# Performance work log

Measured on AMD Instinct MI355X. Metric: run time of the kernel, lower is better.

Reference implementation:

```python
import jax, jax.numpy as jnp
import numpy as np

EC = 64        # n_elts
N = 262144     # number of sample points (2048 rays * 128 samples)


def setup_inputs() -> dict:
    key = jax.random.key(0)
    ks = jax.random.split(key, 7)
    return {
        "world_space_points": jax.random.uniform(ks[0], (N, 3), minval=-0.7, maxval=0.7, dtype=jnp.float32),
        "nerflet_activations": jax.random.normal(ks[1], (EC, N, 4), dtype=jnp.float32),
        "dists": jax.random.uniform(ks[2], (N, 1), minval=0.0, maxval=0.1, dtype=jnp.float32),
        "constants": jax.random.uniform(ks[3], (EC, 1), minval=5.0, maxval=5.1, dtype=jnp.float32),
        "centers": jax.random.uniform(ks[4], (EC, 3), minval=-0.6, maxval=0.6, dtype=jnp.float32),
        "radii": jax.random.uniform(ks[5], (EC, 3), minval=0.05, maxval=0.06, dtype=jnp.float32),
        "rotations": jax.random.uniform(ks[6], (EC, 3), minval=-np.pi, maxval=np.pi, dtype=jnp.float32),
    }


def _rotation_matrices(rpy):
    # rpy: [EC, 3] roll-pitch-yaw -> [EC, 3, 3]
    c = jnp.cos(rpy)
    s = jnp.sin(rpy)
    cx, cy, cz = c[..., 0], c[..., 1], c[..., 2]
    sx, sy, sz = s[..., 0], s[..., 1], s[..., 2]
    R = jnp.stack([
        cz * cy, cz * sy * sx - sz * cx, cz * sy * cx + sz * sx,
        sz * cy, sz * sy * sx + cz * cx, sz * sy * cx - cz * sx,
        -sy,     cy * sx,                cy * cx,
    ], axis=-1)
    return R.reshape(rpy.shape[:-1] + (3, 3))


def _forward(wsp, act, dists, constants, centers, radii, rotations):
    DIV_EPS = 1e-8
    c = jnp.abs(constants)               # [EC, 1]
    r = jnp.abs(radii) + 0.005           # [EC, 3]
    d = 1.0 / (r + DIV_EPS)              # inverse diagonal
    R = _rotation_matrices(rotations)    # [EC, 3, 3]
    inv_cov = jnp.einsum('eij,ej,ekj->eik', R, d, R)  # R diag(d) R^T

    diff = wsp[None, :, :] - centers[:, None, :]      # [EC, N, 3]
    x, y, z = diff[..., 0], diff[..., 1], diff[..., 2]
    c00 = inv_cov[:, 0, 0][:, None]
    c01 = inv_cov[:, 0, 1][:, None]
    c02 = inv_cov[:, 0, 2][:, None]
    c11 = inv_cov[:, 1, 1][:, None]
    c12 = inv_cov[:, 1, 2][:, None]
    c22 = inv_cov[:, 2, 2][:, None]
    q = (x * (c00 * x + c01 * y + c02 * z)
         + y * (c01 * x + c11 * y + c12 * z)
         + z * (c02 * x + c12 * y + c22 * z))          # [EC, N]
    rbfs = jnp.exp(-0.5 * q)[..., None] * c[:, None, :]  # [EC, N, 1]

    NO_PENALTY_THRESH = 0.01
    penalty = 0.001 * jnp.mean(jnp.sum(jnp.maximum(rbfs - NO_PENALTY_THRESH, 0.0), axis=0))
    bbox_min = jnp.array([[-0.6, -0.6, -0.35]], dtype=wsp.dtype)
    bbox_max = jnp.array([[0.6, 0.6, 0.6]], dtype=wsp.dtype)
    penalty = penalty + jnp.sum(jnp.maximum(centers - bbox_max, 0.0)) \
                      + jnp.sum(jnp.maximum(bbox_min - centers, 0.0))

    # alpha compositing inputs: sigma = last channel, rgb = first 3 channels
    alpha = 1.0 - jnp.exp(-jax.nn.relu(act[..., -1:]) * dists[None])   # [EC, N, 1]
    rgb = jax.nn.sigmoid(act[..., :3])                                  # [EC, N, 3]
    na = jnp.concatenate([rgb, alpha], axis=-1)                         # [EC, N, 4]

    rbf_sums = jnp.sum(rbfs, axis=0, keepdims=True)                     # [1, N, 1]
    KILL_THRESH = 0.0
    out = jnp.where(rbfs < KILL_THRESH, 0.0, rbfs / (rbf_sums + 1e-6) * na)  # [EC, N, 4]
    return jnp.sum(out, axis=0), penalty                                # [N, 4], scalar


def reference(world_space_points, nerflet_activations, dists, constants, centers, radii, rotations):
    return _forward(world_space_points, nerflet_activations, dists,
                    constants, centers, radii, rotations)
```

## Files before the change

### kernel.cpp

```cpp
#include <hip/hip_runtime.h>
#include <math.h>

#define EC_N 64

struct __align__(16) NerfParam {
    float c00, c11, c22, c01_2;
    float c02_2, c12_2, cx, cy;
    float cz, cc, pad0, pad1;
};

__global__ void init_penalty_kernel(const float* __restrict__ centers,
                                    float* __restrict__ pen_out) {
    int e = threadIdx.x;
    float p = 0.f;
    if (e < EC_N) {
        const float bmax[3] = {0.6f, 0.6f, 0.6f};
        const float bmin[3] = {-0.6f, -0.6f, -0.35f};
        #pragma unroll
        for (int k = 0; k < 3; ++k) {
            float cv = centers[e * 3 + k];
            p += fmaxf(cv - bmax[k], 0.f) + fmaxf(bmin[k] - cv, 0.f);
        }
    }
    #pragma unroll
    for (int off = 32; off > 0; off >>= 1)
        p += __shfl_down(p, off, 64);
    if (threadIdx.x == 0) *pen_out = p;
}

__global__ __launch_bounds__(256) void rbf_main_kernel(
    const float* __restrict__ wsp,
    const float* __restrict__ act,
    const float* __restrict__ dists,
    const float* __restrict__ constants,
    const float* __restrict__ centers,
    const float* __restrict__ radii,
    const float* __restrict__ rotations,
    float* __restrict__ out,
    float* __restrict__ pen,
    int n)
{
    __shared__ NerfParam sp[EC_N];
    __shared__ float s_pen[4];

    const int tid = threadIdx.x;

    if (tid < EC_N) {
        const int e = tid;
        float c = fabsf(constants[e]);
        float r0 = fabsf(radii[e * 3 + 0]) + 0.005f;
        float r1 = fabsf(radii[e * 3 + 1]) + 0.005f;
        float r2 = fabsf(radii[e * 3 + 2]) + 0.005f;
        float d0 = 1.f / (r0 + 1e-8f);
        float d1 = 1.f / (r1 + 1e-8f);
        float d2 = 1.f / (r2 + 1e-8f);
        float ax = rotations[e * 3 + 0];
        float ay = rotations[e * 3 + 1];
        float az = rotations[e * 3 + 2];
        float sx, cx, sy, cy, sz, cz;
        sincosf(ax, &sx, &cx);
        sincosf(ay, &sy, &cy);
        sincosf(az, &sz, &cz);
        float R00 = cz * cy;
        float R01 = cz * sy * sx - sz * cx;
        float R02 = cz * sy * cx + sz * sx;
        float R10 = sz * cy;
        float R11 = sz * sy * sx + cz * cx;
        float R12 = sz * sy * cx - cz * sx;
        float R20 = -sy;
        float R21 = cy * sx;
        float R22 = cy * cx;
        float c00 = R00 * R00 * d0 + R01 * R01 * d1 + R02 * R02 * d2;
        float c11 = R10 * R10 * d0 + R11 * R11 * d1 + R12 * R12 * d2;
        float c22 = R20 * R20 * d0 + R21 * R21 * d1 + R22 * R22 * d2;
        float c01 = R00 * R10 * d0 + R01 * R11 * d1 + R02 * R12 * d2;
        float c02 = R00 * R20 * d0 + R01 * R21 * d1 + R02 * R22 * d2;
        float c12 = R10 * R20 * d0 + R11 * R21 * d1 + R12 * R22 * d2;
        NerfParam p;
        p.c00 = c00; p.c11 = c11; p.c22 = c22;
        p.c01_2 = 2.f * c01; p.c02_2 = 2.f * c02; p.c12_2 = 2.f * c12;
        p.cx = centers[e * 3 + 0];
        p.cy = centers[e * 3 + 1];
        p.cz = centers[e * 3 + 2];
        p.cc = c;
        p.pad0 = 0.f; p.pad1 = 0.f;
        sp[e] = p;
    }
    __syncthreads();

    const int i = blockIdx.x * 256 + tid;
    float penLocal = 0.f;

    if (i < n) {
        const float px = wsp[i * 3 + 0];
        const float py = wsp[i * 3 + 1];
        const float pz = wsp[i * 3 + 2];
        const float dist = dists[i];

        float S = 0.f, v0 = 0.f, v1 = 0.f, v2 = 0.f, v3 = 0.f;

        #pragma unroll 8
        for (int e = 0; e < EC_N; ++e) {
            const NerfParam p = sp[e];
            const float x = px - p.cx;
            const float y = py - p.cy;
            const float z = pz - p.cz;
            float q = x * x * p.c00;
            q = fmaf(y * y, p.c11, q);
            q = fmaf(z * z, p.c22, q);
            q = fmaf(x * y, p.c01_2, q);
            q = fmaf(x * z, p.c02_2, q);
            q = fmaf(y * z, p.c12_2, q);
            const float rbf = __expf(-0.5f * q) * p.cc;
            S += rbf;
            penLocal += fmaxf(rbf - 0.01f, 0.f);

            const float4 a = *(const float4*)(act + ((size_t)e * (size_t)n + (size_t)i) * 4);
            const float s0 = 1.f / (1.f + __expf(-a.x));
            const float s1 = 1.f / (1.f + __expf(-a.y));
            const float s2 = 1.f / (1.f + __expf(-a.z));
            const float al = 1.f - __expf(-fmaxf(a.w, 0.f) * dist);
            v0 = fmaf(rbf, s0, v0);
            v1 = fmaf(rbf, s1, v1);
            v2 = fmaf(rbf, s2, v2);
            v3 = fmaf(rbf, al, v3);
        }

        const float inv = 1.f / (S + 1e-6f);
        float4 o;
        o.x = v0 * inv; o.y = v1 * inv; o.z = v2 * inv; o.w = v3 * inv;
        *(float4*)(out + (size_t)i * 4) = o;
    }

    #pragma unroll
    for (int off = 32; off > 0; off >>= 1)
        penLocal += __shfl_down(penLocal, off, 64);
    const int wave = tid >> 6;
    const int lane = tid & 63;
    if (lane == 0) s_pen[wave] = penLocal;
    __syncthreads();
    if (tid == 0) {
        const float t = s_pen[0] + s_pen[1] + s_pen[2] + s_pen[3];
        atomicAdd(pen, t * (0.001f / (float)n));
    }
}

extern "C" void kernel_launch(void* const* d_in, const int* in_sizes, int n_in,
                              void* d_out, int out_size, void* d_ws, size_t ws_size,
                              hipStream_t stream) {
    const float* wsp       = (const float*)d_in[0];
    const float* act       = (const float*)d_in[1];
    const float* dists     = (const float*)d_in[2];
    const float* constants = (const float*)d_in[3];
    const float* centers   = (const float*)d_in[4];
    const float* radii     = (const float*)d_in[5];
    const float* rotations = (const float*)d_in[6];

    const int n = in_sizes[0] / 3;
    float* out = (float*)d_out;
    float* pen = out + (size_t)n * 4;

    init_penalty_kernel<<<1, 64, 0, stream>>>(centers, pen);

    const int blocks = (n + 255) / 256;
    rbf_main_kernel<<<blocks, 256, 0, stream>>>(
        wsp, act, dists, constants, centers, radii, rotations, out, pen, n);
}
```

Measured before the change: 369.7 us.

## Process two points per thread with nontemporal loads and native exp2/rcp

Each thread now handles two sample points, which halves the block count and amortizes the per-block parameter setup and LDS reads. The activation stream is read and the output written with nontemporal hints, and the exponentials and reciprocals use hardware exp2/rcp builtins with log2e folded into the covariance and distance constants. Launch bounds now request two blocks per CU. The kernel is dominated by reading a 268 MB activation tensor, so the benefit depends on whether extra bytes in flight and fewer VALU ops improve bandwidth; native rcp/exp2 carry slightly different accuracy.

```diff
diff --git a/kernel.cpp b/kernel.cpp
--- a/kernel.cpp
+++ b/kernel.cpp
@@ -2,12 +2,19 @@
 #include <math.h>
 
 #define EC_N 64
+#define NEG_HALF_LOG2E (-0.72134752044448170368f)
+#define NEG_LOG2E      (-1.44269504088896340736f)
+
+typedef float v4f __attribute__((ext_vector_type(4)));
 
 struct __align__(16) NerfParam {
     float c00, c11, c22, c01_2;
     float c02_2, c12_2, cx, cy;
     float cz, cc, pad0, pad1;
 };
+
+__device__ __forceinline__ float fast_exp2(float x) { return __builtin_amdgcn_exp2f(x); }
+__device__ __forceinline__ float fast_rcp(float x)  { return __builtin_amdgcn_rcpf(x); }
 
 __global__ void init_penalty_kernel(const float* __restrict__ centers,
                                     float* __restrict__ pen_out) {
@@ -28,7 +35,7 @@
     if (threadIdx.x == 0) *pen_out = p;
 }
 
-__global__ __launch_bounds__(256) void rbf_main_kernel(
+__global__ __launch_bounds__(256, 2) void rbf_main_kernel(
     const float* __restrict__ wsp,
     const float* __restrict__ act,
     const float* __restrict__ dists,
@@ -70,12 +77,13 @@
         float R20 = -sy;
         float R21 = cy * sx;
         float R22 = cy * cx;
-        float c00 = R00 * R00 * d0 + R01 * R01 * d1 + R02 * R02 * d2;
-        float c11 = R10 * R10 * d0 + R11 * R11 * d1 + R12 * R12 * d2;
-        float c22 = R20 * R20 * d0 + R21 * R21 * d1 + R22 * R22 * d2;
-        float c01 = R00 * R10 * d0 + R01 * R11 * d1 + R02 * R12 * d2;
-        float c02 = R00 * R20 * d0 + R01 * R21 * d1 + R02 * R22 * d2;
-        float c12 = R10 * R20 * d0 + R11 * R21 * d1 + R12 * R22 * d2;
+        const float k = NEG_HALF_LOG2E;
+        float c00 = (R00 * R00 * d0 + R01 * R01 * d1 + R02 * R02 * d2) * k;
+        float c11 = (R10 * R10 * d0 + R11 * R11 * d1 + R12 * R12 * d2) * k;
+        float c22 = (R20 * R20 * d0 + R21 * R21 * d1 + R22 * R22 * d2) * k;
+        float c01 = (R00 * R10 * d0 + R01 * R11 * d1 + R02 * R12 * d2) * k;
+        float c02 = (R00 * R20 * d0 + R01 * R21 * d1 + R02 * R22 * d2) * k;
+        float c12 = (R10 * R20 * d0 + R11 * R21 * d1 + R12 * R22 * d2) * k;
         NerfParam p;
         p.c00 = c00; p.c11 = c11; p.c22 = c22;
         p.c01_2 = 2.f * c01; p.c02_2 = 2.f * c02; p.c12_2 = 2.f * c12;
@@ -88,50 +96,85 @@
     }
     __syncthreads();
 
-    const int i = blockIdx.x * 256 + tid;
-    float penLocal = 0.f;
-
-    if (i < n) {
-        const float px = wsp[i * 3 + 0];
-        const float py = wsp[i * 3 + 1];
-        const float pz = wsp[i * 3 + 2];
-        const float dist = dists[i];
-
-        float S = 0.f, v0 = 0.f, v1 = 0.f, v2 = 0.f, v3 = 0.f;
-
-        #pragma unroll 8
-        for (int e = 0; e < EC_N; ++e) {
-            const NerfParam p = sp[e];
-            const float x = px - p.cx;
-            const float y = py - p.cy;
-            const float z = pz - p.cz;
+    const int i0 = blockIdx.x * 512 + tid;
+    const int i1 = i0 + 256;
+    const bool ok0 = i0 < n;
+    const bool ok1 = i1 < n;
+    const int j0 = ok0 ? i0 : 0;
+    const int j1 = ok1 ? i1 : 0;
+
+    const float px0 = wsp[j0 * 3 + 0], py0 = wsp[j0 * 3 + 1], pz0 = wsp[j0 * 3 + 2];
+    const float px1 = wsp[j1 * 3 + 0], py1 = wsp[j1 * 3 + 1], pz1 = wsp[j1 * 3 + 2];
+    const float dl0 = dists[j0] * NEG_LOG2E;
+    const float dl1 = dists[j1] * NEG_LOG2E;
+
+    const v4f* pa0 = (const v4f*)act + j0;
+    const v4f* pa1 = (const v4f*)act + j1;
+
+    float S0 = 0.f, u0 = 0.f, u1 = 0.f, u2 = 0.f, u3 = 0.f, pen0 = 0.f;
+    float S1 = 0.f, w0 = 0.f, w1 = 0.f, w2 = 0.f, w3 = 0.f, pen1 = 0.f;
+
+    #pragma unroll 8
+    for (int e = 0; e < EC_N; ++e) {
+        const NerfParam p = sp[e];
+
+        const v4f a0 = __builtin_nontemporal_load(pa0); pa0 += n;
+        const v4f a1 = __builtin_nontemporal_load(pa1); pa1 += n;
+
+        {
+            const float x = px0 - p.cx, y = py0 - p.cy, z = pz0 - p.cz;
             float q = x * x * p.c00;
             q = fmaf(y * y, p.c11, q);
             q = fmaf(z * z, p.c22, q);
             q = fmaf(x * y, p.c01_2, q);
             q = fmaf(x * z, p.c02_2, q);
             q = fmaf(y * z, p.c12_2, q);
-            const float rbf = __expf(-0.5f * q) * p.cc;
-            S += rbf;
-            penLocal += fmaxf(rbf - 0.01f, 0.f);
-
-            const float4 a = *(const float4*)(act + ((size_t)e * (size_t)n + (size_t)i) * 4);
-            const float s0 = 1.f / (1.f + __expf(-a.x));
-            const float s1 = 1.f / (1.f + __expf(-a.y));
-            const float s2 = 1.f / (1.f + __expf(-a.z));
-            const float al = 1.f - __expf(-fmaxf(a.w, 0.f) * dist);
-            v0 = fmaf(rbf, s0, v0);
-            v1 = fmaf(rbf, s1, v1);
-            v2 = fmaf(rbf, s2, v2);
-            v3 = fmaf(rbf, al, v3);
+            const float rbf = fast_exp2(q) * p.cc;
+            S0 += rbf;
+            pen0 += fmaxf(rbf - 0.01f, 0.f);
+            const float s0 = fast_rcp(1.f + fast_exp2(a0.x * NEG_LOG2E));
+            const float s1 = fast_rcp(1.f + fast_exp2(a0.y * NEG_LOG2E));
+            const float s2 = fast_rcp(1.f + fast_exp2(a0.z * NEG_LOG2E));
+            const float al = 1.f - fast_exp2(fmaxf(a0.w, 0.f) * dl0);
+            u0 = fmaf(rbf, s0, u0);
+            u1 = fmaf(rbf, s1, u1);
+            u2 = fmaf(rbf, s2, u2);
+            u3 = fmaf(rbf, al, u3);
         }
-
-        const float inv = 1.f / (S + 1e-6f);
-        float4 o;
-        o.x = v0 * inv; o.y = v1 * inv; o.z = v2 * inv; o.w = v3 * inv;
-        *(float4*)(out + (size_t)i * 4) = o;
-    }
-
+        {
+            const float x = px1 - p.cx, y = py1 - p.cy, z = pz1 - p.cz;
+            float q = x * x * p.c00;
+            q = fmaf(y * y, p.c11, q);
+            q = fmaf(z * z, p.c22, q);
+            q = fmaf(x * y, p.c01_2, q);
+            q = fmaf(x * z, p.c02_2, q);
+            q = fmaf(y * z, p.c12_2, q);
+            const float rbf = fast_exp2(q) * p.cc;
+            S1 += rbf;
+            pen1 += fmaxf(rbf - 0.01f, 0.f);
+            const float s0 = fast_rcp(1.f + fast_exp2(a1.x * NEG_LOG2E));
+            const float s1 = fast_rcp(1.f + fast_exp2(a1.y * NEG_LOG2E));
+            const float s2 = fast_rcp(1.f + fast_exp2(a1.z * NEG_LOG2E));
+            const float al = 1.f - fast_exp2(fmaxf(a1.w, 0.f) * dl1);
+            w0 = fmaf(rbf, s0, w0);
+            w1 = fmaf(rbf, s1, w1);
+            w2 = fmaf(rbf, s2, w2);
+            w3 = fmaf(rbf, al, w3);
+        }
+    }
+
+    if (ok0) {
+        const float inv = fast_rcp(S0 + 1e-6f);
+        v4f o; o.x = u0 * inv; o.y = u1 * inv; o.z = u2 * inv; o.w = u3 * inv;
+        __builtin_nontemporal_store(o, (v4f*)out + i0);
+    }
+    if (ok1) {
+        const float inv = fast_rcp(S1 + 1e-6f);
+        v4f o; o.x = w0 * inv; o.y = w1 * inv; o.z = w2 * inv; o.w = w3 * inv;
+        __builtin_nontemporal_store(o, (v4f*)out + i1);
+    }
+
+    float penLocal = (ok0 ? pen0 : 0.f) + (ok1 ? pen1 : 0.f);
     #pragma unroll
     for (int off = 32; off > 0; off >>= 1)
         penLocal += __shfl_down(penLocal, off, 64);
@@ -162,7 +205,7 @@
 
     init_penalty_kernel<<<1, 64, 0, stream>>>(centers, pen);
 
-    const int blocks = (n + 255) / 256;
+    const int blocks = (n + 511) / 512;
     rbf_main_kernel<<<blocks, 256, 0, stream>>>(
         wsp, act, dists, constants, centers, radii, rotations, out, pen, n);
 }
```

New measurement: 360.5 us. 2.5% less time.

## Software-pipeline activation loads across two element streams with nontemporal access and exp2 math

Applied to the files above, without the earlier changes.

Splits the 64-element loop into two interleaved streams (elements e and e+32), each with double-buffered nontemporal float4 loads of activations issued ahead of use, so more memory requests are in flight per thread. Folds -0.5*log2(e) into the covariance coefficients and uses hardware exp2/rcp intrinsics to cut transcendental instruction count. Output is written with a nontemporal store, and launch bounds request 4 blocks per CU. The prefetch buffers add register pressure, and the approximate rcp/exp2 intrinsics slightly change numerics.

```diff
diff --git a/kernel.cpp b/kernel.cpp
--- a/kernel.cpp
+++ b/kernel.cpp
@@ -2,12 +2,20 @@
 #include <math.h>
 
 #define EC_N 64
+#define NEG_HALF_LOG2E (-0.72134752044448170368f)
+#define NEG_LOG2E      (-1.44269504088896340736f)
+
+typedef float v4f __attribute__((ext_vector_type(4)));
 
 struct __align__(16) NerfParam {
     float c00, c11, c22, c01_2;
     float c02_2, c12_2, cx, cy;
     float cz, cc, pad0, pad1;
 };
+
+__device__ __forceinline__ float fast_exp2(float x) { return __builtin_amdgcn_exp2f(x); }
+__device__ __forceinline__ float fast_rcp(float x)  { return __builtin_amdgcn_rcpf(x); }
+__device__ __forceinline__ v4f nt_load(const v4f* p) { return __builtin_nontemporal_load(p); }
 
 __global__ void init_penalty_kernel(const float* __restrict__ centers,
                                     float* __restrict__ pen_out) {
@@ -28,7 +36,7 @@
     if (threadIdx.x == 0) *pen_out = p;
 }
 
-__global__ __launch_bounds__(256) void rbf_main_kernel(
+__global__ __launch_bounds__(256, 4) void rbf_main_kernel(
     const float* __restrict__ wsp,
     const float* __restrict__ act,
     const float* __restrict__ dists,
@@ -70,12 +78,13 @@
         float R20 = -sy;
         float R21 = cy * sx;
         float R22 = cy * cx;
-        float c00 = R00 * R00 * d0 + R01 * R01 * d1 + R02 * R02 * d2;
-        float c11 = R10 * R10 * d0 + R11 * R11 * d1 + R12 * R12 * d2;
-        float c22 = R20 * R20 * d0 + R21 * R21 * d1 + R22 * R22 * d2;
-        float c01 = R00 * R10 * d0 + R01 * R11 * d1 + R02 * R12 * d2;
-        float c02 = R00 * R20 * d0 + R01 * R21 * d1 + R02 * R22 * d2;
-        float c12 = R10 * R20 * d0 + R11 * R21 * d1 + R12 * R22 * d2;
+        const float k = NEG_HALF_LOG2E;
+        float c00 = (R00 * R00 * d0 + R01 * R01 * d1 + R02 * R02 * d2) * k;
+        float c11 = (R10 * R10 * d0 + R11 * R11 * d1 + R12 * R12 * d2) * k;
+        float c22 = (R20 * R20 * d0 + R21 * R21 * d1 + R22 * R22 * d2) * k;
+        float c01 = (R00 * R10 * d0 + R01 * R11 * d1 + R02 * R12 * d2) * k;
+        float c02 = (R00 * R20 * d0 + R01 * R21 * d1 + R02 * R22 * d2) * k;
+        float c12 = (R10 * R20 * d0 + R11 * R21 * d1 + R12 * R22 * d2) * k;
         NerfParam p;
         p.c00 = c00; p.c11 = c11; p.c22 = c22;
         p.c01_2 = 2.f * c01; p.c02_2 = 2.f * c02; p.c12_2 = 2.f * c12;
@@ -89,49 +98,84 @@
     __syncthreads();
 
     const int i = blockIdx.x * 256 + tid;
-    float penLocal = 0.f;
-
-    if (i < n) {
-        const float px = wsp[i * 3 + 0];
-        const float py = wsp[i * 3 + 1];
-        const float pz = wsp[i * 3 + 2];
-        const float dist = dists[i];
-
-        float S = 0.f, v0 = 0.f, v1 = 0.f, v2 = 0.f, v3 = 0.f;
-
-        #pragma unroll 8
-        for (int e = 0; e < EC_N; ++e) {
+    const bool ok = i < n;
+    const int j = ok ? i : 0;
+
+    const float px = wsp[j * 3 + 0];
+    const float py = wsp[j * 3 + 1];
+    const float pz = wsp[j * 3 + 2];
+    const float dl = dists[j] * NEG_LOG2E;
+
+    const v4f* plo = (const v4f*)act + j;
+    const v4f* phi = (const v4f*)act + ((size_t)32 * n + j);
+
+    v4f A0 = nt_load(plo); plo += n;
+    v4f B0 = nt_load(phi); phi += n;
+    v4f A1 = nt_load(plo); plo += n;
+    v4f B1 = nt_load(phi); phi += n;
+
+    float S = 0.f, v0 = 0.f, v1 = 0.f, v2 = 0.f, v3 = 0.f, penL = 0.f;
+
+    #pragma unroll 2
+    for (int e = 0; e < 32; ++e) {
+        const v4f aLo = A0; A0 = A1;
+        const v4f aHi = B0; B0 = B1;
+        if (e < 30) {
+            A1 = nt_load(plo); plo += n;
+            B1 = nt_load(phi); phi += n;
+        }
+
+        {
             const NerfParam p = sp[e];
-            const float x = px - p.cx;
-            const float y = py - p.cy;
-            const float z = pz - p.cz;
+            const float x = px - p.cx, y = py - p.cy, z = pz - p.cz;
             float q = x * x * p.c00;
             q = fmaf(y * y, p.c11, q);
             q = fmaf(z * z, p.c22, q);
             q = fmaf(x * y, p.c01_2, q);
             q = fmaf(x * z, p.c02_2, q);
             q = fmaf(y * z, p.c12_2, q);
-            const float rbf = __expf(-0.5f * q) * p.cc;
+            const float rbf = fast_exp2(q) * p.cc;
             S += rbf;
-            penLocal += fmaxf(rbf - 0.01f, 0.f);
-
-            const float4 a = *(const float4*)(act + ((size_t)e * (size_t)n + (size_t)i) * 4);
-            const float s0 = 1.f / (1.f + __expf(-a.x));
-            const float s1 = 1.f / (1.f + __expf(-a.y));
-            const float s2 = 1.f / (1.f + __expf(-a.z));
-            const float al = 1.f - __expf(-fmaxf(a.w, 0.f) * dist);
+            penL += fmaxf(rbf - 0.01f, 0.f);
+            const float s0 = fast_rcp(1.f + fast_exp2(aLo.x * NEG_LOG2E));
+            const float s1 = fast_rcp(1.f + fast_exp2(aLo.y * NEG_LOG2E));
+            const float s2 = fast_rcp(1.f + fast_exp2(aLo.z * NEG_LOG2E));
+            const float al = 1.f - fast_exp2(fmaxf(aLo.w, 0.f) * dl);
             v0 = fmaf(rbf, s0, v0);
             v1 = fmaf(rbf, s1, v1);
             v2 = fmaf(rbf, s2, v2);
             v3 = fmaf(rbf, al, v3);
         }
-
-        const float inv = 1.f / (S + 1e-6f);
-        float4 o;
-        o.x = v0 * inv; o.y = v1 * inv; o.z = v2 * inv; o.w = v3 * inv;
-        *(float4*)(out + (size_t)i * 4) = o;
-    }
-
+        {
+            const NerfParam p = sp[e + 32];
+            const float x = px - p.cx, y = py - p.cy, z = pz - p.cz;
+            float q = x * x * p.c00;
+            q = fmaf(y * y, p.c11, q);
+            q = fmaf(z * z, p.c22, q);
+            q = fmaf(x * y, p.c01_2, q);
+            q = fmaf(x * z, p.c02_2, q);
+            q = fmaf(y * z, p.c12_2, q);
+            const float rbf = fast_exp2(q) * p.cc;
+            S += rbf;
+            penL += fmaxf(rbf - 0.01f, 0.f);
+            const float s0 = fast_rcp(1.f + fast_exp2(aHi.x * NEG_LOG2E));
+            const float s1 = fast_rcp(1.f + fast_exp2(aHi.y * NEG_LOG2E));
+            const float s2 = fast_rcp(1.f + fast_exp2(aHi.z * NEG_LOG2E));
+            const float al = 1.f - fast_exp2(fmaxf(aHi.w, 0.f) * dl);
+            v0 = fmaf(rbf, s0, v0);
+            v1 = fmaf(rbf, s1, v1);
+            v2 = fmaf(rbf, s2, v2);
+            v3 = fmaf(rbf, al, v3);
+        }
+    }
+
+    if (ok) {
+        const float inv = fast_rcp(S + 1e-6f);
+        v4f o; o.x = v0 * inv; o.y = v1 * inv; o.z = v2 * inv; o.w = v3 * inv;
+        __builtin_nontemporal_store(o, (v4f*)out + i);
+    }
+
+    float penLocal = ok ? penL : 0.f;
     #pragma unroll
     for (int off = 32; off > 0; off >>= 1)
         penLocal += __shfl_down(penLocal, off, 64);
```

New measurement: 356.6 us. -3.5%, faster.

## Process four points per thread with double-buffered nontemporal activation loads

Applied to the files above, without the earlier changes.

Each thread now handles four sample points. The activation rows for the next nerflet are prefetched two iterations ahead into register double buffers using nontemporal loads. The -0.5*log2e scale is folded into the inverse-covariance coefficients so the RBF uses a raw exp2 builtin, and the sigmoids use exp2 plus hardware reciprocal. This is meant to hide memory latency on the 268MB activation stream and cut per-exp ALU work. In exchange it raises register pressure (launch bounds 256,2) and launches four times fewer blocks.

```diff
diff --git a/kernel.cpp b/kernel.cpp
--- a/kernel.cpp
+++ b/kernel.cpp
@@ -2,12 +2,21 @@
 #include <math.h>
 
 #define EC_N 64
+#define NEG_HALF_LOG2E (-0.72134752044448170368f)
+#define NEG_LOG2E      (-1.44269504088896340736f)
+#define PTS_PER_THREAD 4
+
+typedef float v4f __attribute__((ext_vector_type(4)));
 
 struct __align__(16) NerfParam {
     float c00, c11, c22, c01_2;
     float c02_2, c12_2, cx, cy;
     float cz, cc, pad0, pad1;
 };
+
+__device__ __forceinline__ float fast_exp2(float x) { return __builtin_amdgcn_exp2f(x); }
+__device__ __forceinline__ float fast_rcp(float x)  { return __builtin_amdgcn_rcpf(x); }
+__device__ __forceinline__ v4f nt_load(const v4f* p) { return __builtin_nontemporal_load(p); }
 
 __global__ void init_penalty_kernel(const float* __restrict__ centers,
                                     float* __restrict__ pen_out) {
@@ -28,7 +37,7 @@
     if (threadIdx.x == 0) *pen_out = p;
 }
 
-__global__ __launch_bounds__(256) void rbf_main_kernel(
+__global__ __launch_bounds__(256, 2) void rbf_main_kernel(
     const float* __restrict__ wsp,
     const float* __restrict__ act,
     const float* __restrict__ dists,
@@ -70,12 +79,13 @@
         float R20 = -sy;
         float R21 = cy * sx;
         float R22 = cy * cx;
-        float c00 = R00 * R00 * d0 + R01 * R01 * d1 + R02 * R02 * d2;
-        float c11 = R10 * R10 * d0 + R11 * R11 * d1 + R12 * R12 * d2;
-        float c22 = R20 * R20 * d0 + R21 * R21 * d1 + R22 * R22 * d2;
-        float c01 = R00 * R10 * d0 + R01 * R11 * d1 + R02 * R12 * d2;
-        float c02 = R00 * R20 * d0 + R01 * R21 * d1 + R02 * R22 * d2;
-        float c12 = R10 * R20 * d0 + R11 * R21 * d1 + R12 * R22 * d2;
+        const float k = NEG_HALF_LOG2E;
+        float c00 = (R00 * R00 * d0 + R01 * R01 * d1 + R02 * R02 * d2) * k;
+        float c11 = (R10 * R10 * d0 + R11 * R11 * d1 + R12 * R12 * d2) * k;
+        float c22 = (R20 * R20 * d0 + R21 * R21 * d1 + R22 * R22 * d2) * k;
+        float c01 = (R00 * R10 * d0 + R01 * R11 * d1 + R02 * R12 * d2) * k;
+        float c02 = (R00 * R20 * d0 + R01 * R21 * d1 + R02 * R22 * d2) * k;
+        float c12 = (R10 * R20 * d0 + R11 * R21 * d1 + R12 * R22 * d2) * k;
         NerfParam p;
         p.c00 = c00; p.c11 = c11; p.c22 = c22;
         p.c01_2 = 2.f * c01; p.c02_2 = 2.f * c02; p.c12_2 = 2.f * c12;
@@ -88,50 +98,91 @@
     }
     __syncthreads();
 
-    const int i = blockIdx.x * 256 + tid;
-    float penLocal = 0.f;
-
-    if (i < n) {
-        const float px = wsp[i * 3 + 0];
-        const float py = wsp[i * 3 + 1];
-        const float pz = wsp[i * 3 + 2];
-        const float dist = dists[i];
-
-        float S = 0.f, v0 = 0.f, v1 = 0.f, v2 = 0.f, v3 = 0.f;
-
-        #pragma unroll 8
-        for (int e = 0; e < EC_N; ++e) {
-            const NerfParam p = sp[e];
-            const float x = px - p.cx;
-            const float y = py - p.cy;
-            const float z = pz - p.cz;
+    const int base = blockIdx.x * (256 * PTS_PER_THREAD) + tid;
+    int   idx[PTS_PER_THREAD];
+    bool  okk[PTS_PER_THREAD];
+    float px[PTS_PER_THREAD], py[PTS_PER_THREAD], pz[PTS_PER_THREAD], dl[PTS_PER_THREAD];
+    #pragma unroll
+    for (int k = 0; k < PTS_PER_THREAD; ++k) {
+        const int i = base + k * 256;
+        okk[k] = i < n;
+        idx[k] = okk[k] ? i : 0;
+        px[k] = wsp[idx[k] * 3 + 0];
+        py[k] = wsp[idx[k] * 3 + 1];
+        pz[k] = wsp[idx[k] * 3 + 2];
+        dl[k] = dists[idx[k]] * NEG_LOG2E;
+    }
+
+    const v4f* pact = (const v4f*)act;
+
+    v4f buf0[PTS_PER_THREAD], buf1[PTS_PER_THREAD];
+    #pragma unroll
+    for (int k = 0; k < PTS_PER_THREAD; ++k)
+        buf0[k] = nt_load(pact + (size_t)0 * n + idx[k]);
+    #pragma unroll
+    for (int k = 0; k < PTS_PER_THREAD; ++k)
+        buf1[k] = nt_load(pact + (size_t)1 * n + idx[k]);
+
+    float S[PTS_PER_THREAD], v0[PTS_PER_THREAD], v1[PTS_PER_THREAD],
+          v2[PTS_PER_THREAD], v3[PTS_PER_THREAD];
+    #pragma unroll
+    for (int k = 0; k < PTS_PER_THREAD; ++k) {
+        S[k] = 0.f; v0[k] = 0.f; v1[k] = 0.f; v2[k] = 0.f; v3[k] = 0.f;
+    }
+    float penL = 0.f;
+
+    #pragma unroll 2
+    for (int e = 0; e < EC_N; ++e) {
+        v4f a[PTS_PER_THREAD];
+        const bool even = (e & 1) == 0;
+        #pragma unroll
+        for (int k = 0; k < PTS_PER_THREAD; ++k)
+            a[k] = even ? buf0[k] : buf1[k];
+
+        if (e < EC_N - 2) {
+            const v4f* row = pact + (size_t)(e + 2) * n;
+            #pragma unroll
+            for (int k = 0; k < PTS_PER_THREAD; ++k) {
+                const v4f t = nt_load(row + idx[k]);
+                if (even) buf0[k] = t; else buf1[k] = t;
+            }
+        }
+
+        const NerfParam p = sp[e];
+        #pragma unroll
+        for (int k = 0; k < PTS_PER_THREAD; ++k) {
+            const float x = px[k] - p.cx, y = py[k] - p.cy, z = pz[k] - p.cz;
             float q = x * x * p.c00;
             q = fmaf(y * y, p.c11, q);
             q = fmaf(z * z, p.c22, q);
             q = fmaf(x * y, p.c01_2, q);
             q = fmaf(x * z, p.c02_2, q);
             q = fmaf(y * z, p.c12_2, q);
-            const float rbf = __expf(-0.5f * q) * p.cc;
-            S += rbf;
-            penLocal += fmaxf(rbf - 0.01f, 0.f);
-
-            const float4 a = *(const float4*)(act + ((size_t)e * (size_t)n + (size_t)i) * 4);
-            const float s0 = 1.f / (1.f + __expf(-a.x));
-            const float s1 = 1.f / (1.f + __expf(-a.y));
-            const float s2 = 1.f / (1.f + __expf(-a.z));
-            const float al = 1.f - __expf(-fmaxf(a.w, 0.f) * dist);
-            v0 = fmaf(rbf, s0, v0);
-            v1 = fmaf(rbf, s1, v1);
-            v2 = fmaf(rbf, s2, v2);
-            v3 = fmaf(rbf, al, v3);
-        }
-
-        const float inv = 1.f / (S + 1e-6f);
-        float4 o;
-        o.x = v0 * inv; o.y = v1 * inv; o.z = v2 * inv; o.w = v3 * inv;
-        *(float4*)(out + (size_t)i * 4) = o;
-    }
-
+            const float rbf = fast_exp2(q) * p.cc;
+            S[k] += rbf;
+            penL += okk[k] ? fmaxf(rbf - 0.01f, 0.f) : 0.f;
+            const float s0 = fast_rcp(1.f + fast_exp2(a[k].x * NEG_LOG2E));
+            const float s1 = fast_rcp(1.f + fast_exp2(a[k].y * NEG_LOG2E));
+            const float s2 = fast_rcp(1.f + fast_exp2(a[k].z * NEG_LOG2E));
+            const float al = 1.f - fast_exp2(fmaxf(a[k].w, 0.f) * dl[k]);
+            v0[k] = fmaf(rbf, s0, v0[k]);
+            v1[k] = fmaf(rbf, s1, v1[k]);
+            v2[k] = fmaf(rbf, s2, v2[k]);
+            v3[k] = fmaf(rbf, al, v3[k]);
+        }
+    }
+
+    #pragma unroll
+    for (int k = 0; k < PTS_PER_THREAD; ++k) {
+        if (okk[k]) {
+            const float inv = fast_rcp(S[k] + 1e-6f);
+            v4f o;
+            o.x = v0[k] * inv; o.y = v1[k] * inv; o.z = v2[k] * inv; o.w = v3[k] * inv;
+            __builtin_nontemporal_store(o, (v4f*)out + idx[k]);
+        }
+    }
+
+    float penLocal = penL;
     #pragma unroll
     for (int off = 32; off > 0; off >>= 1)
         penLocal += __shfl_down(penLocal, off, 64);
@@ -162,7 +213,8 @@
 
     init_penalty_kernel<<<1, 64, 0, stream>>>(centers, pen);
 
-    const int blocks = (n + 255) / 256;
+    const int pts_per_block = 256 * PTS_PER_THREAD;
+    const int blocks = (n + pts_per_block - 1) / pts_per_block;
     rbf_main_kernel<<<blocks, 256, 0, stream>>>(
         wsp, act, dists, constants, centers, radii, rotations, out, pen, n);
 }
```

After: 357.4 us. 3.3% less time.
